# Optimization experiments

Hardware: AMD Instinct MI355X
Metric: run time of the kernel (lower is better)

Reference implementation:

```python
import jax, jax.numpy as jnp
import numpy as np

N_NODES = 50000
N_EDGES = 800000
IN = 64
HID = 64
OUT = 12
N_LAYERS = 4
N_GRAPHS = 512


def setup_inputs() -> dict:
    key = jax.random.key(0)
    ks = jax.random.split(key, 20)
    s = 1.0 / np.sqrt(HID)
    inp = {
        "x": jax.random.normal(ks[0], (N_NODES, IN), dtype=jnp.float32),
        "edge_index": jax.random.randint(ks[1], (2, N_EDGES), 0, N_NODES, dtype=jnp.int32),
        "batch": jnp.sort(jax.random.randint(ks[2], (N_NODES,), 0, N_GRAPHS, dtype=jnp.int32)),
        "batch_size": N_GRAPHS,
        # stacked per-layer ResGatedGraphConv params (in == hidden so one stack works)
        "Wk": jax.random.normal(ks[3], (N_LAYERS, HID, HID), dtype=jnp.float32) * s,
        "bk": jnp.zeros((N_LAYERS, HID), dtype=jnp.float32),
        "Wq": jax.random.normal(ks[4], (N_LAYERS, HID, HID), dtype=jnp.float32) * s,
        "bq": jnp.zeros((N_LAYERS, HID), dtype=jnp.float32),
        "Wv": jax.random.normal(ks[5], (N_LAYERS, HID, HID), dtype=jnp.float32) * s,
        "bv": jnp.zeros((N_LAYERS, HID), dtype=jnp.float32),
        "Ws": jax.random.normal(ks[6], (N_LAYERS, HID, HID), dtype=jnp.float32) * s,
        "bs": jnp.zeros((N_LAYERS, HID), dtype=jnp.float32),
        "mlp_w1": jax.random.normal(ks[7], (HID, HID), dtype=jnp.float32) * s,
        "mlp_b1": jnp.zeros((HID,), dtype=jnp.float32),
        "mlp_w2": jax.random.normal(ks[8], (HID, OUT), dtype=jnp.float32) * s,
        "mlp_b2": jnp.zeros((OUT,), dtype=jnp.float32),
    }
    return inp


def _res_gated_conv(x, src, dst, wk, bk_, wq, bq_, wv, bv_, ws, bs_, n_nodes):
    # PyG ResGatedGraphConv: eta = sigmoid(key(x_i) + query(x_j)); agg_i = sum eta * value(x_j)
    k = x @ wk + bk_  # [N, H]
    q = x @ wq + bq_
    v = x @ wv + bv_
    gate = jax.nn.sigmoid(k[dst] + q[src])          # [E, H] gather + elementwise
    msg = gate * v[src]                              # [E, H]
    agg = jax.ops.segment_sum(msg, dst, num_segments=n_nodes)  # scatter-add
    return agg + x @ ws + bs_                        # root/skip connection


def reference(x, edge_index, batch, batch_size, Wk, bk, Wq, bq, Wv, bv, Ws, bs,
              mlp_w1, mlp_b1, mlp_w2, mlp_b2):
    src, dst = edge_index[0], edge_index[1]  # messages flow src(j) -> dst(i)
    n_nodes = x.shape[0]
    for l in range(N_LAYERS):
        x = _res_gated_conv(x, src, dst, Wk[l], bk[l], Wq[l], bq[l],
                            Wv[l], bv[l], Ws[l], bs[l], n_nodes)
        x = jax.nn.gelu(x, approximate=False)  # torch nn.GELU default = exact
    # global mean pool over graphs
    sums = jax.ops.segment_sum(x, batch, num_segments=batch_size)          # [B, H]
    cnts = jax.ops.segment_sum(jnp.ones((n_nodes,), x.dtype), batch,
                               num_segments=batch_size)                    # [B]
    pooled = sums / jnp.maximum(cnts, 1.0)[:, None]
    # MLP head: Linear -> ReLU -> (dropout off at inference) -> Linear
    h = jax.nn.relu(pooled @ mlp_w1 + mlp_b1)
    return h @ mlp_w2 + mlp_b2
```

## Files before the change

### kernel.cpp

```cpp
#include <hip/hip_runtime.h>
#include <math.h>

#define N_NODES  50000
#define N_EDGES  800000
#define HID      64
#define OUT_DIM  12
#define N_LAYERS 4
#define N_GRAPHS 512

#define SCAN_CHUNK 512
#define N_CHUNKS   ((N_NODES + SCAN_CHUNK - 1) / SCAN_CHUNK)

typedef unsigned short u16;
typedef unsigned int   u32;
typedef __attribute__((ext_vector_type(8))) short bf16x8;
typedef __attribute__((ext_vector_type(4))) float f32x4;

__device__ __forceinline__ u32 f2bf(float f) {
    u32 u = __float_as_uint(f);
    return (u + 0x7FFFu + ((u >> 16) & 1u)) >> 16;
}
__device__ __forceinline__ float bf2f(u32 h) {
    return __uint_as_float(h << 16);
}

__global__ __launch_bounds__(256) void wprep_kernel(
    const float* __restrict__ Wq, const float* __restrict__ Wv,
    const float* __restrict__ Wk, const float* __restrict__ Ws,
    u16* __restrict__ wt)
{
    int m = blockIdx.x;
    int lyr = m >> 2, j = m & 3;
    const float* src;
    switch (j) { case 0: src = Wq; break; case 1: src = Wv; break;
                 case 2: src = Wk; break; default: src = Ws; }
    src += (size_t)lyr * HID * HID;
    int t  = threadIdx.x;
    int n  = t >> 2;
    int k0 = (t & 3) * 16;
    u32 buf[8];
    #pragma unroll
    for (int i = 0; i < 16; i += 2) {
        float f0 = src[(k0 + i) * HID + n];
        float f1 = src[(k0 + i + 1) * HID + n];
        buf[i / 2] = f2bf(f0) | (f2bf(f1) << 16);
    }
    u32* dst = (u32*)(wt + (size_t)m * 4096 + n * 64 + k0);
    *(uint4*)(dst)     = make_uint4(buf[0], buf[1], buf[2], buf[3]);
    *(uint4*)(dst + 4) = make_uint4(buf[4], buf[5], buf[6], buf[7]);
}

__global__ __launch_bounds__(256) void cvt_kernel(
    const float* __restrict__ x, u32* __restrict__ xbf)
{
    int i = blockIdx.x * 256 + threadIdx.x;
    if (i >= N_NODES * HID / 8) return;
    float4 a = ((const float4*)x)[2 * i];
    float4 b = ((const float4*)x)[2 * i + 1];
    ((uint4*)xbf)[i] = make_uint4(
        f2bf(a.x) | (f2bf(a.y) << 16), f2bf(a.z) | (f2bf(a.w) << 16),
        f2bf(b.x) | (f2bf(b.y) << 16), f2bf(b.z) | (f2bf(b.w) << 16));
}

__global__ __launch_bounds__(256) void gemm_mfma_kernel(
    const u16* __restrict__ xbf, const u16* __restrict__ wt, int layer,
    const float* __restrict__ bq, const float* __restrict__ bv,
    const float* __restrict__ bk, const float* __restrict__ bs,
    u32* __restrict__ qv, float* __restrict__ ok, float* __restrict__ os)
{
    const int t = threadIdx.x;
    const int w = t >> 6;
    const int l = t & 63;
    const int row16 = l & 15;
    const int kgrp  = l >> 4;
    const int gbase = blockIdx.x * 64;

    const u16 *wA, *wB; const float *bA, *bB;
    if (blockIdx.y == 0) { wA = wt + (size_t)(layer * 4 + 0) * 4096; bA = bq;
                           wB = wt + (size_t)(layer * 4 + 1) * 4096; bB = bv; }
    else                 { wA = wt + (size_t)(layer * 4 + 2) * 4096; bA = bk;
                           wB = wt + (size_t)(layer * 4 + 3) * 4096; bB = bs; }

    int nodeA = gbase + w * 16 + row16;
    int nodeAc = nodeA < N_NODES ? nodeA : N_NODES - 1;
    bf16x8 a0 = *(const bf16x8*)(xbf + (size_t)nodeAc * 64 + kgrp * 8);
    bf16x8 a1 = *(const bf16x8*)(xbf + (size_t)nodeAc * 64 + 32 + kgrp * 8);

    f32x4 acc[2][4];
    #pragma unroll
    for (int nt = 0; nt < 4; ++nt) {
        float fa = bA[nt * 16 + row16];
        float fb = bB[nt * 16 + row16];
        acc[0][nt] = (f32x4){fa, fa, fa, fa};
        acc[1][nt] = (f32x4){fb, fb, fb, fb};
    }

    #pragma unroll
    for (int nt = 0; nt < 4; ++nt) {
        const u16* pa = wA + (nt * 16 + row16) * 64 + kgrp * 8;
        const u16* pb = wB + (nt * 16 + row16) * 64 + kgrp * 8;
        bf16x8 ba0 = *(const bf16x8*)(pa);
        bf16x8 ba1 = *(const bf16x8*)(pa + 32);
        bf16x8 bb0 = *(const bf16x8*)(pb);
        bf16x8 bb1 = *(const bf16x8*)(pb + 32);
        acc[0][nt] = __builtin_amdgcn_mfma_f32_16x16x32_bf16(a0, ba0, acc[0][nt], 0, 0, 0);
        acc[0][nt] = __builtin_amdgcn_mfma_f32_16x16x32_bf16(a1, ba1, acc[0][nt], 0, 0, 0);
        acc[1][nt] = __builtin_amdgcn_mfma_f32_16x16x32_bf16(a0, bb0, acc[1][nt], 0, 0, 0);
        acc[1][nt] = __builtin_amdgcn_mfma_f32_16x16x32_bf16(a1, bb1, acc[1][nt], 0, 0, 0);
    }

    if (blockIdx.y == 0) {
        #pragma unroll
        for (int nt = 0; nt < 4; ++nt) {
            #pragma unroll
            for (int r = 0; r < 4; ++r) {
                float qe = acc[0][nt][r];
                float qo = __shfl_xor(qe, 1);
                float ve = acc[1][nt][r];
                float vo = __shfl_xor(ve, 1);
                if (!(l & 1)) {
                    int gn = gbase + w * 16 + kgrp * 4 + r;
                    if (gn < N_NODES) {
                        u32 qp = f2bf(qe) | (f2bf(qo) << 16);
                        u32 vp = f2bf(ve) | (f2bf(vo) << 16);
                        *(uint2*)(qv + (size_t)gn * 64 + nt * 16 + row16) = make_uint2(qp, vp);
                    }
                }
            }
        }
    } else {
        #pragma unroll
        for (int nt = 0; nt < 4; ++nt) {
            #pragma unroll
            for (int r = 0; r < 4; ++r) {
                int gn = gbase + w * 16 + kgrp * 4 + r;
                if (gn < N_NODES) {
                    int col = nt * 16 + row16;
                    ok[(size_t)gn * 64 + col] = acc[0][nt][r];
                    os[(size_t)gn * 64 + col] = acc[1][nt][r];
                }
            }
        }
    }
}

__global__ __launch_bounds__(256) void hist_kernel(
    const int* __restrict__ ei, int* __restrict__ deg, int* __restrict__ rank)
{
    int e0 = (blockIdx.x * 256 + threadIdx.x) * 4;
    #pragma unroll
    for (int i = 0; i < 4; ++i) {
        int e = e0 + i;
        if (e < N_EDGES) rank[e] = atomicAdd(&deg[ei[N_EDGES + e]], 1);
    }
}

__global__ __launch_bounds__(SCAN_CHUNK) void scan1_kernel(
    const int* __restrict__ deg, int* __restrict__ base, int* __restrict__ blocksum)
{
    __shared__ int s[SCAN_CHUNK];
    int t = threadIdx.x;
    int i = blockIdx.x * SCAN_CHUNK + t;
    int v = (i < N_NODES) ? deg[i] : 0;
    s[t] = v;
    __syncthreads();
    for (int off = 1; off < SCAN_CHUNK; off <<= 1) {
        int u = (t >= off) ? s[t - off] : 0;
        __syncthreads();
        s[t] += u;
        __syncthreads();
    }
    if (i < N_NODES) base[i] = s[t] - v;
    if (t == SCAN_CHUNK - 1) blocksum[blockIdx.x] = s[t];
}

__global__ __launch_bounds__(128) void scan2_kernel(
    const int* __restrict__ blocksum, int* __restrict__ blockoff)
{
    __shared__ int s[128];
    int t = threadIdx.x;
    int v = (t < N_CHUNKS) ? blocksum[t] : 0;
    s[t] = v;
    __syncthreads();
    for (int off = 1; off < 128; off <<= 1) {
        int u = (t >= off) ? s[t - off] : 0;
        __syncthreads();
        s[t] += u;
        __syncthreads();
    }
    if (t < N_CHUNKS) blockoff[t] = s[t] - v;
}

__global__ __launch_bounds__(SCAN_CHUNK) void scan3_kernel(
    int* __restrict__ base, const int* __restrict__ blockoff)
{
    int i = blockIdx.x * SCAN_CHUNK + threadIdx.x;
    if (i < N_NODES) base[i] += blockoff[blockIdx.x];
    if (i == 0) base[N_NODES] = N_EDGES;
}

__global__ __launch_bounds__(256) void scatter_kernel(
    const int* __restrict__ ei, const int* __restrict__ base,
    const int* __restrict__ rank, int* __restrict__ csr_src)
{
    int e0 = (blockIdx.x * 256 + threadIdx.x) * 4;
    #pragma unroll
    for (int i = 0; i < 4; ++i) {
        int e = e0 + i;
        if (e < N_EDGES)
            csr_src[base[ei[N_EDGES + e]] + rank[e]] = ei[e];
    }
}

__global__ __launch_bounds__(256) void agg_gelu_kernel(
    const int* __restrict__ base, const int* __restrict__ csr_src,
    const float* __restrict__ kf, const u32* __restrict__ qv,
    const float* __restrict__ skip, u32* __restrict__ outxbf)
{
    int node = blockIdx.x * 4 + (threadIdx.x >> 6);
    if (node >= N_NODES) return;
    int lane = threadIdx.x & 63;
    int half = lane >> 5;
    int c    = lane & 31;

    float2 kd = *(const float2*)(kf + (size_t)node * HID + 2 * c);
    float acc0 = 0.f, acc1 = 0.f;
    int p0 = base[node];
    int p1 = base[node + 1];

    #pragma unroll 2
    for (int p = p0 + half; p < p1; p += 2) {
        int s = csr_src[p];
        uint2 qp = *(const uint2*)(qv + (size_t)s * 64 + 2 * c);
        float q0 = bf2f(qp.x & 0xffffu), q1 = bf2f(qp.x >> 16);
        float v0 = bf2f(qp.y & 0xffffu), v1 = bf2f(qp.y >> 16);
        float g0 = 1.f / (1.f + __expf(-(kd.x + q0)));
        float g1 = 1.f / (1.f + __expf(-(kd.y + q1)));
        acc0 = fmaf(g0, v0, acc0);
        acc1 = fmaf(g1, v1, acc1);
    }

    acc0 += __shfl_xor(acc0, 32);
    acc1 += __shfl_xor(acc1, 32);

    if (half == 0) {
        float2 sk = *(const float2*)(skip + (size_t)node * HID + 2 * c);
        float xo0 = acc0 + sk.x;
        float xo1 = acc1 + sk.y;
        float g0 = 0.5f * xo0 * (1.f + erff(xo0 * 0.70710678118f));
        float g1 = 0.5f * xo1 * (1.f + erff(xo1 * 0.70710678118f));
        outxbf[(size_t)node * 32 + c] = f2bf(g0) | (f2bf(g1) << 16);
    }
}

__global__ __launch_bounds__(256) void bounds_kernel(
    const int* __restrict__ batch, int* __restrict__ start)
{
    int n = blockIdx.x * 256 + threadIdx.x;
    if (n >= N_NODES) return;
    int b  = batch[n];
    int bp = (n == 0) ? -1 : batch[n - 1];
    for (int g = bp + 1; g <= b; ++g) start[g] = n;
    if (n == N_NODES - 1) {
        for (int g = b + 1; g <= N_GRAPHS; ++g) start[g] = N_NODES;
    }
}

__global__ __launch_bounds__(256) void pool2_kernel(
    const u32* __restrict__ xbf, const int* __restrict__ start,
    float* __restrict__ pooled)
{
    int g   = blockIdx.x;
    int t   = threadIdx.x;
    int nid = t >> 5;
    int c   = t & 31;
    int s0 = start[g];
    int s1 = start[g + 1];
    float a0 = 0.f, a1 = 0.f;
    for (int n = s0 + nid; n < s1; n += 8) {
        u32 p = xbf[(size_t)n * 32 + c];
        a0 += bf2f(p & 0xffffu);
        a1 += bf2f(p >> 16);
    }
    __shared__ float red0[8][32], red1[8][32];
    red0[nid][c] = a0; red1[nid][c] = a1;
    __syncthreads();
    if (nid == 0) {
        float t0 = 0.f, t1 = 0.f;
        #pragma unroll
        for (int i = 0; i < 8; ++i) { t0 += red0[i][c]; t1 += red1[i][c]; }
        float cnt = fmaxf((float)(s1 - s0), 1.f);
        *(float2*)(pooled + (size_t)g * HID + 2 * c) = make_float2(t0 / cnt, t1 / cnt);
    }
}

__global__ __launch_bounds__(64) void head_kernel(
    const float* __restrict__ pooled,
    const float* __restrict__ w1, const float* __restrict__ b1,
    const float* __restrict__ w2, const float* __restrict__ b2,
    float* __restrict__ out)
{
    int g = blockIdx.x;
    int t = threadIdx.x;
    __shared__ float p[64];
    __shared__ float h[64];
    p[t] = pooled[(size_t)g * HID + t];
    __syncthreads();
    float acc = b1[t];
    #pragma unroll 8
    for (int k = 0; k < HID; ++k) acc = fmaf(p[k], w1[k * HID + t], acc);
    h[t] = fmaxf(acc, 0.f);
    __syncthreads();
    if (t < OUT_DIM) {
        float a2 = b2[t];
        #pragma unroll 8
        for (int k = 0; k < HID; ++k) a2 = fmaf(h[k], w2[k * OUT_DIM + t], a2);
        out[(size_t)g * OUT_DIM + t] = a2;
    }
}

extern "C" void kernel_launch(void* const* d_in, const int* in_sizes, int n_in,
                              void* d_out, int out_size, void* d_ws, size_t ws_size,
                              hipStream_t stream)
{
    const float* x     = (const float*)d_in[0];
    const int*   ei    = (const int*)d_in[1];
    const int*   batch = (const int*)d_in[2];
    const float* Wk = (const float*)d_in[4];
    const float* bk = (const float*)d_in[5];
    const float* Wq = (const float*)d_in[6];
    const float* bq = (const float*)d_in[7];
    const float* Wv = (const float*)d_in[8];
    const float* bv = (const float*)d_in[9];
    const float* Ws = (const float*)d_in[10];
    const float* bs = (const float*)d_in[11];
    const float* w1 = (const float*)d_in[12];
    const float* b1 = (const float*)d_in[13];
    const float* w2 = (const float*)d_in[14];
    const float* b2 = (const float*)d_in[15];
    float* out = (float*)d_out;

    char* wsb = (char*)d_ws;
    const size_t NF = (size_t)N_NODES * HID;
    u32*   xbf    = (u32*)wsb;                      wsb += NF * 2;
    float* bufK   = (float*)wsb;                    wsb += NF * 4;
    float* bufS   = (float*)wsb;                    wsb += NF * 4;
    u32*   bufQV  = (u32*)wsb;                      wsb += NF * 4;
    u16*   wt     = (u16*)wsb;                      wsb += (size_t)16 * 4096 * 2;
    float* pooled = (float*)wsb;                    wsb += (size_t)N_GRAPHS * HID * 4;
    int*   baseI  = (int*)wsb;                      wsb += (N_NODES + 1) * 4;
    int*   csr_src= (int*)wsb;                      wsb += (size_t)N_EDGES * 4;
    int*   startI = (int*)wsb;                      wsb += (N_GRAPHS + 1) * 4;
    int* deg      = (int*)bufS;
    int* rank     = deg + N_NODES;
    int* blocksum = rank + N_EDGES;
    int* blockoff = blocksum + 128;

    const int gemm_gx = (N_NODES + 63) / 64;
    const int e4g     = (N_EDGES / 4 + 255) / 256;
    const int agg_gx  = (N_NODES + 3) / 4;
    const int nd_g    = (N_NODES + 255) / 256;
    const int cvt_g   = ((int)(NF / 8) + 255) / 256;

    hipMemsetAsync(deg, 0, (size_t)N_NODES * sizeof(int), stream);
    wprep_kernel<<<16, 256, 0, stream>>>(Wq, Wv, Wk, Ws, wt);
    cvt_kernel<<<cvt_g, 256, 0, stream>>>(x, xbf);
    hist_kernel<<<e4g, 256, 0, stream>>>(ei, deg, rank);
    scan1_kernel<<<N_CHUNKS, SCAN_CHUNK, 0, stream>>>(deg, baseI, blocksum);
    scan2_kernel<<<1, 128, 0, stream>>>(blocksum, blockoff);
    scan3_kernel<<<N_CHUNKS, SCAN_CHUNK, 0, stream>>>(baseI, blockoff);
    scatter_kernel<<<e4g, 256, 0, stream>>>(ei, baseI, rank, csr_src);
    bounds_kernel<<<nd_g, 256, 0, stream>>>(batch, startI);

    for (int l = 0; l < N_LAYERS; ++l) {
        gemm_mfma_kernel<<<dim3(gemm_gx, 2), 256, 0, stream>>>(
            (const u16*)xbf, wt, l,
            bq + (size_t)l * HID, bv + (size_t)l * HID,
            bk + (size_t)l * HID, bs + (size_t)l * HID,
            bufQV, bufK, bufS);
        agg_gelu_kernel<<<agg_gx, 256, 0, stream>>>(
            baseI, csr_src, bufK, bufQV, bufS, xbf);
    }

    pool2_kernel<<<N_GRAPHS, 256, 0, stream>>>(xbf, startI, pooled);
    head_kernel<<<N_GRAPHS, 64, 0, stream>>>(pooled, w1, b1, w2, b2, out);
}
```

Before: 354.0 us.

## Widen aggregation gathers to 16B per lane, store K as bf16, precompute byte offsets

The aggregation kernel now has 16 lanes cover a 64-feature row with 16-byte loads, so four edges are processed per wavefront iteration instead of two. The K projection is stored as bf16 instead of fp32, halving its write and read traffic. The CSR source indices are prescaled to byte offsets, removing the address multiply in the inner loop. This adds an extra cross-lane reduction step and rounds K to bf16, which lowers its precision.

```diff
diff --git a/kernel.cpp b/kernel.cpp
--- a/kernel.cpp
+++ b/kernel.cpp
@@ -22,6 +22,9 @@
 }
 __device__ __forceinline__ float bf2f(u32 h) {
     return __uint_as_float(h << 16);
+}
+__device__ __forceinline__ float bf2f_hi(u32 h) {
+    return __uint_as_float(h & 0xffff0000u);
 }
 
 __global__ __launch_bounds__(256) void wprep_kernel(
@@ -66,7 +69,7 @@
     const u16* __restrict__ xbf, const u16* __restrict__ wt, int layer,
     const float* __restrict__ bq, const float* __restrict__ bv,
     const float* __restrict__ bk, const float* __restrict__ bs,
-    u32* __restrict__ qv, float* __restrict__ ok, float* __restrict__ os)
+    u32* __restrict__ qv, u32* __restrict__ kbf, float* __restrict__ os)
 {
     const int t = threadIdx.x;
     const int w = t >> 6;
@@ -133,11 +136,14 @@
         for (int nt = 0; nt < 4; ++nt) {
             #pragma unroll
             for (int r = 0; r < 4; ++r) {
+                float ke = acc[0][nt][r];
+                float ko = __shfl_xor(ke, 1);
                 int gn = gbase + w * 16 + kgrp * 4 + r;
                 if (gn < N_NODES) {
                     int col = nt * 16 + row16;
-                    ok[(size_t)gn * 64 + col] = acc[0][nt][r];
                     os[(size_t)gn * 64 + col] = acc[1][nt][r];
+                    if (!(l & 1))
+                        kbf[(size_t)gn * 32 + (col >> 1)] = f2bf(ke) | (f2bf(ko) << 16);
                 }
             }
         }
@@ -201,55 +207,62 @@
 
 __global__ __launch_bounds__(256) void scatter_kernel(
     const int* __restrict__ ei, const int* __restrict__ base,
-    const int* __restrict__ rank, int* __restrict__ csr_src)
+    const int* __restrict__ rank, u32* __restrict__ csr_off)
 {
     int e0 = (blockIdx.x * 256 + threadIdx.x) * 4;
     #pragma unroll
     for (int i = 0; i < 4; ++i) {
         int e = e0 + i;
         if (e < N_EDGES)
-            csr_src[base[ei[N_EDGES + e]] + rank[e]] = ei[e];
+            csr_off[base[ei[N_EDGES + e]] + rank[e]] = ((u32)ei[e]) << 8;
     }
 }
 
 __global__ __launch_bounds__(256) void agg_gelu_kernel(
-    const int* __restrict__ base, const int* __restrict__ csr_src,
-    const float* __restrict__ kf, const u32* __restrict__ qv,
+    const int* __restrict__ base, const u32* __restrict__ csr_off,
+    const u32* __restrict__ kbf, const u32* __restrict__ qv,
     const float* __restrict__ skip, u32* __restrict__ outxbf)
 {
     int node = blockIdx.x * 4 + (threadIdx.x >> 6);
     if (node >= N_NODES) return;
-    int lane = threadIdx.x & 63;
-    int half = lane >> 5;
-    int c    = lane & 31;
-
-    float2 kd = *(const float2*)(kf + (size_t)node * HID + 2 * c);
-    float acc0 = 0.f, acc1 = 0.f;
+    int lane  = threadIdx.x & 63;
+    int equad = lane >> 4;
+    int c4    = lane & 15;
+
+    uint2 kp = *(const uint2*)(kbf + (size_t)node * 32 + 2 * c4);
+    float kd0 = bf2f(kp.x & 0xffffu), kd1 = bf2f_hi(kp.x);
+    float kd2 = bf2f(kp.y & 0xffffu), kd3 = bf2f_hi(kp.y);
+
+    float acc0 = 0.f, acc1 = 0.f, acc2 = 0.f, acc3 = 0.f;
     int p0 = base[node];
     int p1 = base[node + 1];
-
-    #pragma unroll 2
-    for (int p = p0 + half; p < p1; p += 2) {
-        int s = csr_src[p];
-        uint2 qp = *(const uint2*)(qv + (size_t)s * 64 + 2 * c);
-        float q0 = bf2f(qp.x & 0xffffu), q1 = bf2f(qp.x >> 16);
-        float v0 = bf2f(qp.y & 0xffffu), v1 = bf2f(qp.y >> 16);
-        float g0 = 1.f / (1.f + __expf(-(kd.x + q0)));
-        float g1 = 1.f / (1.f + __expf(-(kd.y + q1)));
-        acc0 = fmaf(g0, v0, acc0);
-        acc1 = fmaf(g1, v1, acc1);
-    }
-
-    acc0 += __shfl_xor(acc0, 32);
-    acc1 += __shfl_xor(acc1, 32);
-
-    if (half == 0) {
-        float2 sk = *(const float2*)(skip + (size_t)node * HID + 2 * c);
-        float xo0 = acc0 + sk.x;
-        float xo1 = acc1 + sk.y;
-        float g0 = 0.5f * xo0 * (1.f + erff(xo0 * 0.70710678118f));
-        float g1 = 0.5f * xo1 * (1.f + erff(xo1 * 0.70710678118f));
-        outxbf[(size_t)node * 32 + c] = f2bf(g0) | (f2bf(g1) << 16);
+    const char* qvb = (const char*)qv + c4 * 16;
+
+    for (int p = p0 + equad; p < p1; p += 4) {
+        u32 off = csr_off[p];
+        uint4 e = *(const uint4*)(qvb + off);
+        float g;
+        g = 1.f / (1.f + __expf(-(kd0 + bf2f(e.x & 0xffffu)))); acc0 = fmaf(g, bf2f(e.y & 0xffffu), acc0);
+        g = 1.f / (1.f + __expf(-(kd1 + bf2f_hi(e.x))));        acc1 = fmaf(g, bf2f_hi(e.y),        acc1);
+        g = 1.f / (1.f + __expf(-(kd2 + bf2f(e.z & 0xffffu)))); acc2 = fmaf(g, bf2f(e.w & 0xffffu), acc2);
+        g = 1.f / (1.f + __expf(-(kd3 + bf2f_hi(e.z))));        acc3 = fmaf(g, bf2f_hi(e.w),        acc3);
+    }
+
+    acc0 += __shfl_xor(acc0, 16); acc1 += __shfl_xor(acc1, 16);
+    acc2 += __shfl_xor(acc2, 16); acc3 += __shfl_xor(acc3, 16);
+    acc0 += __shfl_xor(acc0, 32); acc1 += __shfl_xor(acc1, 32);
+    acc2 += __shfl_xor(acc2, 32); acc3 += __shfl_xor(acc3, 32);
+
+    if (equad == 0) {
+        float4 sk = *(const float4*)(skip + (size_t)node * HID + 4 * c4);
+        float x0 = acc0 + sk.x, x1 = acc1 + sk.y;
+        float x2 = acc2 + sk.z, x3 = acc3 + sk.w;
+        float g0 = 0.5f * x0 * (1.f + erff(x0 * 0.70710678118f));
+        float g1 = 0.5f * x1 * (1.f + erff(x1 * 0.70710678118f));
+        float g2 = 0.5f * x2 * (1.f + erff(x2 * 0.70710678118f));
+        float g3 = 0.5f * x3 * (1.f + erff(x3 * 0.70710678118f));
+        *(uint2*)(outxbf + (size_t)node * 32 + 2 * c4) =
+            make_uint2(f2bf(g0) | (f2bf(g1) << 16), f2bf(g2) | (f2bf(g3) << 16));
     }
 }
 
@@ -343,13 +356,13 @@
     char* wsb = (char*)d_ws;
     const size_t NF = (size_t)N_NODES * HID;
     u32*   xbf    = (u32*)wsb;                      wsb += NF * 2;
-    float* bufK   = (float*)wsb;                    wsb += NF * 4;
+    u32*   bufK   = (u32*)wsb;                      wsb += NF * 2;
     float* bufS   = (float*)wsb;                    wsb += NF * 4;
     u32*   bufQV  = (u32*)wsb;                      wsb += NF * 4;
     u16*   wt     = (u16*)wsb;                      wsb += (size_t)16 * 4096 * 2;
     float* pooled = (float*)wsb;                    wsb += (size_t)N_GRAPHS * HID * 4;
     int*   baseI  = (int*)wsb;                      wsb += (N_NODES + 1) * 4;
-    int*   csr_src= (int*)wsb;                      wsb += (size_t)N_EDGES * 4;
+    u32*   csr_off= (u32*)wsb;                      wsb += (size_t)N_EDGES * 4;
     int*   startI = (int*)wsb;                      wsb += (N_GRAPHS + 1) * 4;
     int* deg      = (int*)bufS;
     int* rank     = deg + N_NODES;
@@ -369,7 +382,7 @@
     scan1_kernel<<<N_CHUNKS, SCAN_CHUNK, 0, stream>>>(deg, baseI, blocksum);
     scan2_kernel<<<1, 128, 0, stream>>>(blocksum, blockoff);
     scan3_kernel<<<N_CHUNKS, SCAN_CHUNK, 0, stream>>>(baseI, blockoff);
-    scatter_kernel<<<e4g, 256, 0, stream>>>(ei, baseI, rank, csr_src);
+    scatter_kernel<<<e4g, 256, 0, stream>>>(ei, baseI, rank, csr_off);
     bounds_kernel<<<nd_g, 256, 0, stream>>>(batch, startI);
 
     for (int l = 0; l < N_LAYERS; ++l) {
@@ -379,7 +392,7 @@
             bk + (size_t)l * HID, bs + (size_t)l * HID,
             bufQV, bufK, bufS);
         agg_gelu_kernel<<<agg_gx, 256, 0, stream>>>(
-            baseI, csr_src, bufK, bufQV, bufS, xbf);
+            baseI, csr_off, bufK, bufQV, bufS, xbf);
     }
 
     pool2_kernel<<<N_GRAPHS, 256, 0, stream>>>(xbf, startI, pooled);
```

New measurement: 362.4 us. 1.02x slower.
